# Kernel optimization log

Measured on AMD Instinct MI355X. Metric: run time of the kernel, lower is better.

The kernel has to match this reference:

```python
import jax, jax.numpy as jnp
import numpy as np

B, S, D, H, K = 8, 1024, 512, 512, 8  # batch, seq, input_dim, hidden, max neighbors


def setup_inputs() -> dict:
    key = jax.random.key(0)
    ks = jax.random.split(key, 10)
    p = lambda k, shape: (0.05 * jax.random.normal(k, shape, jnp.float32))
    return {
        "input_t": jax.random.normal(ks[0], (B, S, D), jnp.float32),
        "comb_idx": jax.random.randint(ks[1], (B, S, K), 0, S, jnp.int32),
        "comb_mask": jax.random.randint(ks[2], (B, S, K), 0, 2, jnp.int32),
        "order": jnp.arange(B, dtype=jnp.int64),
        # PyTorch LSTM params per direction; b = b_ih + b_hh fused (mathematically identical)
        "w_ih_f": p(ks[3], (4 * H, D)),
        "w_hh_f": p(ks[4], (4 * H, H)),
        "b_f": p(ks[5], (4 * H,)),
        "w_ih_b": p(ks[6], (4 * H, D)),
        "w_hh_b": p(ks[7], (4 * H, H)),
        "b_b": p(ks[8], (4 * H,)),
    }


def _lstm_scan(x_sbd, w_ih, w_hh, b, reverse):
    # x_sbd: [S, B, D]; PyTorch gate order i, f, g, o; zero initial state (inithidden)
    Bb = x_sbd.shape[1]
    Hh = w_hh.shape[1]
    h0 = jnp.zeros((Bb, Hh), x_sbd.dtype)
    c0 = jnp.zeros((Bb, Hh), x_sbd.dtype)

    def cell(carry, xt):
        h, c = carry
        z = xt @ w_ih.T + h @ w_hh.T + b
        i, f, g, o = jnp.split(z, 4, axis=-1)
        c = jax.nn.sigmoid(f) * c + jax.nn.sigmoid(i) * jnp.tanh(g)
        h = jax.nn.sigmoid(o) * jnp.tanh(c)
        return (h, c), h

    (hn, cn), hs = jax.lax.scan(cell, (h0, c0), x_sbd, reverse=reverse)
    return hs, hn, cn  # hs in original time order even when reverse=True


def reference(input_t, comb_idx, comb_mask, order, w_ih_f, w_hh_f, b_f, w_ih_b, w_hh_b, b_b):
    x = jnp.swapaxes(input_t, 0, 1)  # [S, B, D]
    hs_f, hn_f, cn_f = _lstm_scan(x, w_ih_f, w_hh_f, b_f, reverse=False)
    hs_b, hn_b, cn_b = _lstm_scan(x, w_ih_b, w_hh_b, b_b, reverse=True)
    padded = jnp.swapaxes(jnp.concatenate([hs_f, hs_b], axis=-1), 0, 1)  # [B, S, 2H]
    h_n = jnp.stack([hn_f, hn_b])  # [2, B, H]
    c_n = jnp.stack([cn_f, cn_b])

    # comb = batch_comb[order[idx]]
    ci = comb_idx[order]                                  # [B, S, K]
    cm = comb_mask[order].astype(padded.dtype)            # [B, S, K]
    gathered = jax.vmap(lambda xb, ib: xb[ib])(padded, ci)  # [B, S, K, 2H]
    neigh_sum = (gathered * cm[..., None]).sum(axis=2)    # [B, S, 2H]
    cnt = cm.sum(axis=-1)                                 # [B, S]
    rep = (padded + neigh_sum) / (1.0 + cnt)[..., None]   # (x_i + sum_j x_j) / (|comb_i| + 1)
    rep = rep[:, 1:-1, :]                                 # drop first/last token

    # reorder_batch_encoder_rep[order[i]] = rep[i]
    out = jnp.zeros_like(rep).at[order].set(rep)
    return out, h_n, c_n
```

## Files before the change

### kernel.cpp

```cpp
#include <hip/hip_runtime.h>
#include <stdint.h>

typedef unsigned short u16;
typedef unsigned long long u64;
typedef __attribute__((ext_vector_type(8))) short short8v;
typedef __attribute__((ext_vector_type(4))) float f32x4;

#define OUT_HN   8372224
#define OUT_CN   8380416

#define WS_WIH0  0
#define WS_WIH1  (WS_WIH0 + 2097152)
#define WS_WHH0  (WS_WIH1 + 2097152)
#define WS_WHH1  (WS_WHH0 + 2097152)
#define WS_HSB0  (WS_WHH1 + 2097152)
#define WS_HSB1  (WS_HSB0 + 8396800)
#define WS_FLAGS (WS_HSB1 + 8396800)

__device__ __forceinline__ u16 f2bf(float f) {
  uint32_t u = __float_as_uint(f);
  u += 0x7FFFu + ((u >> 16) & 1u);
  return (u16)(u >> 16);
}
__device__ __forceinline__ float bf2f(u16 v) {
  return __uint_as_float(((uint32_t)v) << 16);
}

__global__ void k_f2bf(const float* __restrict__ src, u16* __restrict__ dst, int n) {
  int i = blockIdx.x * blockDim.x + threadIdx.x;
  int stride = gridDim.x * blockDim.x;
  for (; i < n; i += stride) dst[i] = f2bf(src[i]);
}

__global__ void k_init(uint32_t* flags) {
  if (threadIdx.x < 64) flags[threadIdx.x] = 0;
}

__launch_bounds__(256, 1)
__global__ void k_lstm(const float* __restrict__ xf,
                       const u16* __restrict__ wih0, const u16* __restrict__ wih1,
                       const u16* __restrict__ whh0, const u16* __restrict__ whh1,
                       const float* __restrict__ bias0, const float* __restrict__ bias1,
                       u16* hsb0, u16* hsb1, float* out, uint32_t* flags)
{
  const int tid  = threadIdx.x;
  const int wid  = tid >> 6;
  const int lane = tid & 63;
  const int dir  = blockIdx.x >> 4;
  const int wg   = blockIdx.x & 15;
  const int jbase = wg * 32;

  const u16*  wih  = dir ? wih1  : wih0;
  const u16*  whh  = dir ? whh1  : whh0;
  const float* bias = dir ? bias1 : bias0;
  u16* hsb = dir ? hsb1 : hsb0;
  uint32_t* fl = flags + dir * 16;

  __shared__ u16 hL[8 * 512];
  __shared__ u16 xL[8 * 512];
  __shared__ float zL[4 * 8 * 32];
  __shared__ u16 hS[8 * 32];

  short8v bih[2][16], bhh[2][16];
  {
    const int rr = lane & 15;
    const int ko = (lane >> 4) * 8;
    #pragma unroll
    for (int nt = 0; nt < 2; ++nt) {
      const int row = wid * 512 + jbase + nt * 16 + rr;
      #pragma unroll
      for (int kt = 0; kt < 16; ++kt) {
        bih[nt][kt] = *(const short8v*)(wih + (size_t)row * 512 + kt * 32 + ko);
        bhh[nt][kt] = *(const short8v*)(whh + (size_t)row * 512 + kt * 32 + ko);
      }
    }
  }

  const int cb = tid >> 5;
  const int cj = tid & 31;
  float c_state = 0.f;
  const float bz0 = bias[0 * 512 + jbase + cj];
  const float bz1 = bias[1 * 512 + jbase + cj];
  const float bz2 = bias[2 * 512 + jbase + cj];
  const float bz3 = bias[3 * 512 + jbase + cj];

  const int rB = lane & 7;
  const int q  = lane >> 4;

  const f32x4 fzero = {0.f, 0.f, 0.f, 0.f};
  f32x4 acc0 = fzero, acc1 = fzero;

  #define STAGE_X(tcol)                                                        \
    {                                                                          \
      _Pragma("unroll")                                                        \
      for (int half = 0; half < 2; ++half) {                                   \
        int g = tid + half * 256;                                              \
        int r = g >> 6, B = g & 63;                                            \
        const float* xr = xf + ((size_t)r * 1024 + (tcol)) * 512 + B * 8;      \
        float4 a = *(const float4*)xr;                                         \
        float4 b = *(const float4*)(xr + 4);                                   \
        short8v v;                                                             \
        v[0] = (short)f2bf(a.x); v[1] = (short)f2bf(a.y);                      \
        v[2] = (short)f2bf(a.z); v[3] = (short)f2bf(a.w);                      \
        v[4] = (short)f2bf(b.x); v[5] = (short)f2bf(b.y);                      \
        v[6] = (short)f2bf(b.z); v[7] = (short)f2bf(b.w);                      \
        *(short8v*)(xL + r * 512 + ((B ^ r) << 3)) = v;                        \
      }                                                                        \
    }

  {
    const int t0 = dir ? 1023 : 0;
    STAGE_X(t0);
    __syncthreads();
    #pragma unroll
    for (int kt = 0; kt < 16; ++kt) {
      short8v ax = *(const short8v*)(xL + rB * 512 + (((kt * 4 + q) ^ rB) << 3));
      acc0 = __builtin_amdgcn_mfma_f32_16x16x32_bf16(ax, bih[0][kt], acc0, 0, 0, 0);
      acc1 = __builtin_amdgcn_mfma_f32_16x16x32_bf16(ax, bih[1][kt], acc1, 0, 0, 0);
    }
  }

  for (int step = 0; step < 1024; ++step) {
    if (step > 0) {
      if (tid < 16) {
        int guard = 0;
        while (__hip_atomic_load(&fl[tid], __ATOMIC_RELAXED, __HIP_MEMORY_SCOPE_AGENT)
               < (uint32_t)step && ++guard < (1 << 15)) { }
      }
      __syncthreads();
      {
        const u64* hc = (const u64*)(hsb + (size_t)step * 4096);
        u64 d0 = __hip_atomic_load(hc + 4 * tid + 0, __ATOMIC_RELAXED, __HIP_MEMORY_SCOPE_AGENT);
        u64 d1 = __hip_atomic_load(hc + 4 * tid + 1, __ATOMIC_RELAXED, __HIP_MEMORY_SCOPE_AGENT);
        u64 d2 = __hip_atomic_load(hc + 4 * tid + 2, __ATOMIC_RELAXED, __HIP_MEMORY_SCOPE_AGENT);
        u64 d3 = __hip_atomic_load(hc + 4 * tid + 3, __ATOMIC_RELAXED, __HIP_MEMORY_SCOPE_AGENT);
        union { u64 qq[2]; short8v v; } p0, p1;
        p0.qq[0] = d0; p0.qq[1] = d1;
        p1.qq[0] = d2; p1.qq[1] = d3;
        int G0 = 2 * tid, G1 = 2 * tid + 1;
        int r0 = G0 >> 6, B0 = G0 & 63;
        int r1 = G1 >> 6, B1 = G1 & 63;
        *(short8v*)(hL + r0 * 512 + ((B0 ^ r0) << 3)) = p0.v;
        *(short8v*)(hL + r1 * 512 + ((B1 ^ r1) << 3)) = p1.v;
      }
      __syncthreads();
      #pragma unroll
      for (int kt = 0; kt < 16; ++kt) {
        short8v ah = *(const short8v*)(hL + rB * 512 + (((kt * 4 + q) ^ rB) << 3));
        acc0 = __builtin_amdgcn_mfma_f32_16x16x32_bf16(ah, bhh[0][kt], acc0, 0, 0, 0);
        acc1 = __builtin_amdgcn_mfma_f32_16x16x32_bf16(ah, bhh[1][kt], acc1, 0, 0, 0);
      }
    }
    if (lane < 32) {
      #pragma unroll
      for (int r = 0; r < 4; ++r) {
        const int brow = (lane >> 4) * 4 + r;
        zL[wid * 256 + brow * 32 + (lane & 15)]      = acc0[r];
        zL[wid * 256 + brow * 32 + 16 + (lane & 15)] = acc1[r];
      }
    }
    __syncthreads();
    {
      float zi = zL[0 * 256 + cb * 32 + cj] + bz0;
      float zf = zL[1 * 256 + cb * 32 + cj] + bz1;
      float zg = zL[2 * 256 + cb * 32 + cj] + bz2;
      float zo = zL[3 * 256 + cb * 32 + cj] + bz3;
      float si = 1.f / (1.f + __expf(-zi));
      float sf = 1.f / (1.f + __expf(-zf));
      float so = 1.f / (1.f + __expf(-zo));
      float ag = fabsf(zg); float eg = __expf(-2.f * ag);
      float tg = (1.f - eg) / (1.f + eg); tg = copysignf(tg, zg);
      c_state = sf * c_state + si * tg;
      float ac = fabsf(c_state); float ec = __expf(-2.f * ac);
      float tc = (1.f - ec) / (1.f + ec); tc = copysignf(tc, c_state);
      float h = so * tc;
      hS[cb * 32 + cj] = f2bf(h);
      if (step == 1023) {
        out[OUT_HN + dir * 4096 + cb * 512 + jbase + cj] = h;
        out[OUT_CN + dir * 4096 + cb * 512 + jbase + cj] = c_state;
      }
    }
    __syncthreads();
    if (tid < 64) {
      const int pb = tid >> 3;
      const int pt = tid & 7;
      u64 hv = *(const u64*)(hS + pb * 32 + 4 * pt);
      u64* dst = (u64*)(hsb + ((size_t)(step + 1) * 8 + pb) * 512 + jbase + 4 * pt);
      __hip_atomic_store(dst, hv, __ATOMIC_RELAXED, __HIP_MEMORY_SCOPE_AGENT);
      asm volatile("s_waitcnt vmcnt(0)" ::: "memory");
    }
    if (tid == 0) {
      __hip_atomic_store(&fl[wg], (uint32_t)(step + 1), __ATOMIC_RELAXED,
                         __HIP_MEMORY_SCOPE_AGENT);
    }
    if (step < 1023) {
      acc0 = fzero; acc1 = fzero;
      const int tn = dir ? (1022 - step) : (step + 1);
      STAGE_X(tn);
      __syncthreads();
      #pragma unroll
      for (int kt = 0; kt < 16; ++kt) {
        short8v ax = *(const short8v*)(xL + rB * 512 + (((kt * 4 + q) ^ rB) << 3));
        acc0 = __builtin_amdgcn_mfma_f32_16x16x32_bf16(ax, bih[0][kt], acc0, 0, 0, 0);
        acc1 = __builtin_amdgcn_mfma_f32_16x16x32_bf16(ax, bih[1][kt], acc1, 0, 0, 0);
      }
    }
  }
}

__global__ void k_combine(const u16* __restrict__ hsb0, const u16* __restrict__ hsb1,
                          const int* __restrict__ cidx, const int* __restrict__ cmask,
                          const int* __restrict__ order, float* __restrict__ out)
{
  const int tid = threadIdx.x;
  const int b = blockIdx.x / 1022;
  const int s = 1 + (blockIdx.x % 1022);
  __shared__ int sidx[8];
  __shared__ float smask[8];
  __shared__ int rsh;
  if (tid == 0) rsh = order[b];
  __syncthreads();
  const int r = rsh;
  if (tid < 8) {
    size_t base = ((size_t)r * 1024 + s) * 8 + tid;
    sidx[tid] = cidx[base];
    smask[tid] = (float)cmask[base];
  }
  __syncthreads();
  float cnt = 0.f;
  #pragma unroll
  for (int k = 0; k < 8; ++k) cnt += smask[k];
  const float inv = 1.f / (1.f + cnt);

  const int col0 = tid * 4;
  const bool isF = col0 < 512;
  const int cloc = isF ? col0 : col0 - 512;
  const u16* hb = isF ? hsb0 : hsb1;

  float v0, v1, v2, v3;
  {
    size_t ci2 = isF ? (size_t)(s + 1) : (size_t)(1024 - s);
    ushort4 qv = *(const ushort4*)(hb + (ci2 * 8 + b) * 512 + cloc);
    v0 = bf2f(qv.x); v1 = bf2f(qv.y); v2 = bf2f(qv.z); v3 = bf2f(qv.w);
  }
  #pragma unroll
  for (int k = 0; k < 8; ++k) {
    float m = smask[k];
    if (m != 0.f) {
      int sp = sidx[k];
      size_t ci2 = isF ? (size_t)(sp + 1) : (size_t)(1024 - sp);
      ushort4 qv = *(const ushort4*)(hb + (ci2 * 8 + b) * 512 + cloc);
      v0 += m * bf2f(qv.x); v1 += m * bf2f(qv.y); v2 += m * bf2f(qv.z); v3 += m * bf2f(qv.w);
    }
  }
  size_t ob = ((size_t)r * 1022 + (s - 1)) * 1024 + col0;
  float4 ov; ov.x = v0 * inv; ov.y = v1 * inv; ov.z = v2 * inv; ov.w = v3 * inv;
  *(float4*)(out + ob) = ov;
}

extern "C" void kernel_launch(void* const* d_in, const int* in_sizes, int n_in,
                              void* d_out, int out_size, void* d_ws, size_t ws_size,
                              hipStream_t stream)
{
  const float* x      = (const float*)d_in[0];
  const int*   cidx   = (const int*)d_in[1];
  const int*   cmask  = (const int*)d_in[2];
  const int*   order  = (const int*)d_in[3];
  const float* wihf = (const float*)d_in[4];
  const float* whhf = (const float*)d_in[5];
  const float* bf   = (const float*)d_in[6];
  const float* wihb = (const float*)d_in[7];
  const float* whhb = (const float*)d_in[8];
  const float* bb   = (const float*)d_in[9];
  float* out = (float*)d_out;

  char* ws = (char*)d_ws;
  u16* WIH0 = (u16*)(ws + WS_WIH0);
  u16* WIH1 = (u16*)(ws + WS_WIH1);
  u16* WHH0 = (u16*)(ws + WS_WHH0);
  u16* WHH1 = (u16*)(ws + WS_WHH1);
  u16* HSB0 = (u16*)(ws + WS_HSB0);
  u16* HSB1 = (u16*)(ws + WS_HSB1);
  uint32_t* FLAGS = (uint32_t*)(ws + WS_FLAGS);

  hipLaunchKernelGGL(k_f2bf, dim3(256), dim3(256), 0, stream, wihf, WIH0, 2048 * 512);
  hipLaunchKernelGGL(k_f2bf, dim3(256), dim3(256), 0, stream, wihb, WIH1, 2048 * 512);
  hipLaunchKernelGGL(k_f2bf, dim3(256), dim3(256), 0, stream, whhf, WHH0, 2048 * 512);
  hipLaunchKernelGGL(k_f2bf, dim3(256), dim3(256), 0, stream, whhb, WHH1, 2048 * 512);
  hipLaunchKernelGGL(k_init, dim3(1), dim3(64), 0, stream, FLAGS);
  hipLaunchKernelGGL(k_lstm, dim3(32), dim3(256), 0, stream,
                     x, WIH0, WIH1, WHH0, WHH1, bf, bb, HSB0, HSB1, out, FLAGS);
  hipLaunchKernelGGL(k_combine, dim3(8 * 1022), dim3(256), 0, stream,
                     HSB0, HSB1, cidx, cmask, order, out);
}
```

Before: 3.353 ms.

## Precompute input projections in parallel kernel, keep only recurrent matmul in sequential loop

Moves the x·W_ih projection out of the sequential LSTM loop into a separate highly parallel kernel (k_zx) that writes bf16 pre-activations to workspace. The recurrent kernel then only does h·W_hh per step plus a small load of the precomputed gates, shortening the critical path per timestep. Weight bf16 conversion kernels are removed and fused into the register loads. It adds a large workspace buffer, bf16 rounding of the input gate contributions, and possibly segmented launches if workspace is small.

```diff
diff --git a/kernel.cpp b/kernel.cpp
--- a/kernel.cpp
+++ b/kernel.cpp
@@ -9,13 +9,11 @@
 #define OUT_HN   8372224
 #define OUT_CN   8380416
 
-#define WS_WIH0  0
-#define WS_WIH1  (WS_WIH0 + 2097152)
-#define WS_WHH0  (WS_WIH1 + 2097152)
-#define WS_WHH1  (WS_WHH0 + 2097152)
-#define WS_HSB0  (WS_WHH1 + 2097152)
-#define WS_HSB1  (WS_HSB0 + 8396800)
-#define WS_FLAGS (WS_HSB1 + 8396800)
+#define WS_FLAGS 0
+#define WS_CSB   4096
+#define WS_HSB0  36864
+#define WS_HSB1  8433664
+#define WS_ZX    16830464
 
 __device__ __forceinline__ u16 f2bf(float f) {
   uint32_t u = __float_as_uint(f);
@@ -25,23 +23,122 @@
 __device__ __forceinline__ float bf2f(u16 v) {
   return __uint_as_float(((uint32_t)v) << 16);
 }
-
-__global__ void k_f2bf(const float* __restrict__ src, u16* __restrict__ dst, int n) {
-  int i = blockIdx.x * blockDim.x + threadIdx.x;
-  int stride = gridDim.x * blockDim.x;
-  for (; i < n; i += stride) dst[i] = f2bf(src[i]);
+__device__ __forceinline__ short8v cvt8(const float* p) {
+  float4 a = *(const float4*)p;
+  float4 b = *(const float4*)(p + 4);
+  short8v r;
+  r[0] = (short)f2bf(a.x); r[1] = (short)f2bf(a.y);
+  r[2] = (short)f2bf(a.z); r[3] = (short)f2bf(a.w);
+  r[4] = (short)f2bf(b.x); r[5] = (short)f2bf(b.y);
+  r[6] = (short)f2bf(b.z); r[7] = (short)f2bf(b.w);
+  return r;
 }
 
 __global__ void k_init(uint32_t* flags) {
   if (threadIdx.x < 64) flags[threadIdx.x] = 0;
 }
 
+__global__ void k_zero(u16* h0, u16* h1, float* c) {
+  int i = blockIdx.x * blockDim.x + threadIdx.x;
+  if (i < 4096) { h0[i] = 0; h1[i] = 0; }
+  if (i < 8192) c[i] = 0.f;
+}
+
+#define STAGE_X(tcol)                                                          \
+  {                                                                            \
+    _Pragma("unroll")                                                          \
+    for (int half = 0; half < 2; ++half) {                                     \
+      int g = tid + half * 256;                                                \
+      int r = g >> 6, B = g & 63;                                              \
+      const float* xr = xf + ((size_t)r * 1024 + (tcol)) * 512 + B * 8;        \
+      float4 a = *(const float4*)xr;                                           \
+      float4 b = *(const float4*)(xr + 4);                                     \
+      short8v v;                                                               \
+      v[0] = (short)f2bf(a.x); v[1] = (short)f2bf(a.y);                        \
+      v[2] = (short)f2bf(a.z); v[3] = (short)f2bf(a.w);                        \
+      v[4] = (short)f2bf(b.x); v[5] = (short)f2bf(b.y);                        \
+      v[6] = (short)f2bf(b.z); v[7] = (short)f2bf(b.w);                        \
+      *(short8v*)(xL + r * 512 + ((B ^ r) << 3)) = v;                          \
+    }                                                                          \
+  }
+
+__global__ void k_zx(const float* __restrict__ xf,
+                     const float* __restrict__ wihf, const float* __restrict__ wihb,
+                     u16* __restrict__ zx, int s0, int seglen)
+{
+  const int nch  = seglen >> 5;
+  const int bid  = blockIdx.x;
+  const int chunk = bid % nch;
+  const int wg   = (bid / nch) & 15;
+  const int dir  = bid / (nch * 16);
+  const int tid  = threadIdx.x;
+  const int wid  = tid >> 6;
+  const int lane = tid & 63;
+  const int jbase = wg * 32;
+  const float* wih = dir ? wihb : wihf;
+
+  __shared__ u16 xL[8 * 512];
+  __shared__ float zL[4 * 8 * 32];
+
+  short8v bih[2][16];
+  {
+    const int rr = lane & 15;
+    const int ko = (lane >> 4) * 8;
+    #pragma unroll
+    for (int nt = 0; nt < 2; ++nt) {
+      const int row = wid * 512 + jbase + nt * 16 + rr;
+      #pragma unroll
+      for (int kt = 0; kt < 16; ++kt)
+        bih[nt][kt] = cvt8(wih + (size_t)row * 512 + kt * 32 + ko);
+    }
+  }
+
+  const int rB = lane & 7;
+  const int q  = lane >> 4;
+  const f32x4 fzero = {0.f, 0.f, 0.f, 0.f};
+
+  for (int i = 0; i < 32; ++i) {
+    const int sidx = chunk * 32 + i;
+    const int gstep = s0 + sidx;
+    const int tn = dir ? (1023 - gstep) : gstep;
+    STAGE_X(tn);
+    __syncthreads();
+    f32x4 acc0 = fzero, acc1 = fzero;
+    #pragma unroll
+    for (int kt = 0; kt < 16; ++kt) {
+      short8v ax = *(const short8v*)(xL + rB * 512 + (((kt * 4 + q) ^ rB) << 3));
+      acc0 = __builtin_amdgcn_mfma_f32_16x16x32_bf16(ax, bih[0][kt], acc0, 0, 0, 0);
+      acc1 = __builtin_amdgcn_mfma_f32_16x16x32_bf16(ax, bih[1][kt], acc1, 0, 0, 0);
+    }
+    if (lane < 32) {
+      #pragma unroll
+      for (int r = 0; r < 4; ++r) {
+        const int brow = (lane >> 4) * 4 + r;
+        zL[wid * 256 + brow * 32 + (lane & 15)]      = acc0[r];
+        zL[wid * 256 + brow * 32 + 16 + (lane & 15)] = acc1[r];
+      }
+    }
+    __syncthreads();
+    if (tid < 128) {
+      const int b = tid >> 4;
+      const int r = (tid & 15) * 8;
+      const int g = r >> 5;
+      const int jj = r & 31;
+      short8v v;
+      #pragma unroll
+      for (int w = 0; w < 8; ++w) v[w] = (short)f2bf(zL[g * 256 + b * 32 + jj + w]);
+      *(short8v*)(zx + (((size_t)dir * seglen + sidx) * 16 + wg) * 1024 + tid * 8) = v;
+    }
+    __syncthreads();
+  }
+}
+
 __launch_bounds__(256, 1)
-__global__ void k_lstm(const float* __restrict__ xf,
-                       const u16* __restrict__ wih0, const u16* __restrict__ wih1,
-                       const u16* __restrict__ whh0, const u16* __restrict__ whh1,
+__global__ void k_lstm(const float* __restrict__ whhf, const float* __restrict__ whhb,
                        const float* __restrict__ bias0, const float* __restrict__ bias1,
-                       u16* hsb0, u16* hsb1, float* out, uint32_t* flags)
+                       const u16* __restrict__ zx,
+                       u16* hsb0, u16* hsb1, float* csb, float* out,
+                       uint32_t* flags, int s0, int s1, int seglen)
 {
   const int tid  = threadIdx.x;
   const int wid  = tid >> 6;
@@ -50,18 +147,17 @@
   const int wg   = blockIdx.x & 15;
   const int jbase = wg * 32;
 
-  const u16*  wih  = dir ? wih1  : wih0;
-  const u16*  whh  = dir ? whh1  : whh0;
+  const float* whh  = dir ? whhb : whhf;
   const float* bias = dir ? bias1 : bias0;
   u16* hsb = dir ? hsb1 : hsb0;
   uint32_t* fl = flags + dir * 16;
 
   __shared__ u16 hL[8 * 512];
-  __shared__ u16 xL[8 * 512];
   __shared__ float zL[4 * 8 * 32];
   __shared__ u16 hS[8 * 32];
-
-  short8v bih[2][16], bhh[2][16];
+  __shared__ u64 zxL[256];
+
+  short8v bhh[2][16];
   {
     const int rr = lane & 15;
     const int ko = (lane >> 4) * 8;
@@ -69,87 +165,58 @@
     for (int nt = 0; nt < 2; ++nt) {
       const int row = wid * 512 + jbase + nt * 16 + rr;
       #pragma unroll
-      for (int kt = 0; kt < 16; ++kt) {
-        bih[nt][kt] = *(const short8v*)(wih + (size_t)row * 512 + kt * 32 + ko);
-        bhh[nt][kt] = *(const short8v*)(whh + (size_t)row * 512 + kt * 32 + ko);
-      }
+      for (int kt = 0; kt < 16; ++kt)
+        bhh[nt][kt] = cvt8(whh + (size_t)row * 512 + kt * 32 + ko);
     }
   }
 
   const int cb = tid >> 5;
   const int cj = tid & 31;
-  float c_state = 0.f;
   const float bz0 = bias[0 * 512 + jbase + cj];
   const float bz1 = bias[1 * 512 + jbase + cj];
   const float bz2 = bias[2 * 512 + jbase + cj];
   const float bz3 = bias[3 * 512 + jbase + cj];
+  float* cp = csb + dir * 4096 + cb * 512 + jbase + cj;
+  float c_state = *cp;
 
   const int rB = lane & 7;
   const int q  = lane >> 4;
-
   const f32x4 fzero = {0.f, 0.f, 0.f, 0.f};
-  f32x4 acc0 = fzero, acc1 = fzero;
-
-  #define STAGE_X(tcol)                                                        \
-    {                                                                          \
-      _Pragma("unroll")                                                        \
-      for (int half = 0; half < 2; ++half) {                                   \
-        int g = tid + half * 256;                                              \
-        int r = g >> 6, B = g & 63;                                            \
-        const float* xr = xf + ((size_t)r * 1024 + (tcol)) * 512 + B * 8;      \
-        float4 a = *(const float4*)xr;                                         \
-        float4 b = *(const float4*)(xr + 4);                                   \
-        short8v v;                                                             \
-        v[0] = (short)f2bf(a.x); v[1] = (short)f2bf(a.y);                      \
-        v[2] = (short)f2bf(a.z); v[3] = (short)f2bf(a.w);                      \
-        v[4] = (short)f2bf(b.x); v[5] = (short)f2bf(b.y);                      \
-        v[6] = (short)f2bf(b.z); v[7] = (short)f2bf(b.w);                      \
-        *(short8v*)(xL + r * 512 + ((B ^ r) << 3)) = v;                        \
-      }                                                                        \
-    }
-
-  {
-    const int t0 = dir ? 1023 : 0;
-    STAGE_X(t0);
-    __syncthreads();
+  const u16* zx16 = (const u16*)zxL;
+
+  for (int gstep = s0; gstep < s1; ++gstep) {
+    {
+      const u64* zp = (const u64*)(zx + (((size_t)dir * seglen + (gstep - s0)) * 16 + wg) * 1024);
+      zxL[tid] = zp[tid];
+    }
+    if (tid < 16) {
+      int guard = 0;
+      while (__hip_atomic_load(&fl[tid], __ATOMIC_RELAXED, __HIP_MEMORY_SCOPE_AGENT)
+             < (uint32_t)gstep && ++guard < (1 << 15)) { }
+    }
+    __syncthreads();
+    {
+      const u64* hc = (const u64*)(hsb + (size_t)gstep * 4096);
+      u64 d0 = __hip_atomic_load(hc + 4 * tid + 0, __ATOMIC_RELAXED, __HIP_MEMORY_SCOPE_AGENT);
+      u64 d1 = __hip_atomic_load(hc + 4 * tid + 1, __ATOMIC_RELAXED, __HIP_MEMORY_SCOPE_AGENT);
+      u64 d2 = __hip_atomic_load(hc + 4 * tid + 2, __ATOMIC_RELAXED, __HIP_MEMORY_SCOPE_AGENT);
+      u64 d3 = __hip_atomic_load(hc + 4 * tid + 3, __ATOMIC_RELAXED, __HIP_MEMORY_SCOPE_AGENT);
+      union { u64 qq[2]; short8v v; } p0, p1;
+      p0.qq[0] = d0; p0.qq[1] = d1;
+      p1.qq[0] = d2; p1.qq[1] = d3;
+      int G0 = 2 * tid, G1 = 2 * tid + 1;
+      int r0 = G0 >> 6, B0 = G0 & 63;
+      int r1 = G1 >> 6, B1 = G1 & 63;
+      *(short8v*)(hL + r0 * 512 + ((B0 ^ r0) << 3)) = p0.v;
+      *(short8v*)(hL + r1 * 512 + ((B1 ^ r1) << 3)) = p1.v;
+    }
+    __syncthreads();
+    f32x4 acc0 = fzero, acc1 = fzero;
     #pragma unroll
     for (int kt = 0; kt < 16; ++kt) {
-      short8v ax = *(const short8v*)(xL + rB * 512 + (((kt * 4 + q) ^ rB) << 3));
-      acc0 = __builtin_amdgcn_mfma_f32_16x16x32_bf16(ax, bih[0][kt], acc0, 0, 0, 0);
-      acc1 = __builtin_amdgcn_mfma_f32_16x16x32_bf16(ax, bih[1][kt], acc1, 0, 0, 0);
-    }
-  }
-
-  for (int step = 0; step < 1024; ++step) {
-    if (step > 0) {
-      if (tid < 16) {
-        int guard = 0;
-        while (__hip_atomic_load(&fl[tid], __ATOMIC_RELAXED, __HIP_MEMORY_SCOPE_AGENT)
-               < (uint32_t)step && ++guard < (1 << 15)) { }
-      }
-      __syncthreads();
-      {
-        const u64* hc = (const u64*)(hsb + (size_t)step * 4096);
-        u64 d0 = __hip_atomic_load(hc + 4 * tid + 0, __ATOMIC_RELAXED, __HIP_MEMORY_SCOPE_AGENT);
-        u64 d1 = __hip_atomic_load(hc + 4 * tid + 1, __ATOMIC_RELAXED, __HIP_MEMORY_SCOPE_AGENT);
-        u64 d2 = __hip_atomic_load(hc + 4 * tid + 2, __ATOMIC_RELAXED, __HIP_MEMORY_SCOPE_AGENT);
-        u64 d3 = __hip_atomic_load(hc + 4 * tid + 3, __ATOMIC_RELAXED, __HIP_MEMORY_SCOPE_AGENT);
-        union { u64 qq[2]; short8v v; } p0, p1;
-        p0.qq[0] = d0; p0.qq[1] = d1;
-        p1.qq[0] = d2; p1.qq[1] = d3;
-        int G0 = 2 * tid, G1 = 2 * tid + 1;
-        int r0 = G0 >> 6, B0 = G0 & 63;
-        int r1 = G1 >> 6, B1 = G1 & 63;
-        *(short8v*)(hL + r0 * 512 + ((B0 ^ r0) << 3)) = p0.v;
-        *(short8v*)(hL + r1 * 512 + ((B1 ^ r1) << 3)) = p1.v;
-      }
-      __syncthreads();
-      #pragma unroll
-      for (int kt = 0; kt < 16; ++kt) {
-        short8v ah = *(const short8v*)(hL + rB * 512 + (((kt * 4 + q) ^ rB) << 3));
-        acc0 = __builtin_amdgcn_mfma_f32_16x16x32_bf16(ah, bhh[0][kt], acc0, 0, 0, 0);
-        acc1 = __builtin_amdgcn_mfma_f32_16x16x32_bf16(ah, bhh[1][kt], acc1, 0, 0, 0);
-      }
+      short8v ah = *(const short8v*)(hL + rB * 512 + (((kt * 4 + q) ^ rB) << 3));
+      acc0 = __builtin_amdgcn_mfma_f32_16x16x32_bf16(ah, bhh[0][kt], acc0, 0, 0, 0);
+      acc1 = __builtin_amdgcn_mfma_f32_16x16x32_bf16(ah, bhh[1][kt], acc1, 0, 0, 0);
     }
     if (lane < 32) {
       #pragma unroll
@@ -161,10 +228,10 @@
     }
     __syncthreads();
     {
-      float zi = zL[0 * 256 + cb * 32 + cj] + bz0;
-      float zf = zL[1 * 256 + cb * 32 + cj] + bz1;
-      float zg = zL[2 * 256 + cb * 32 + cj] + bz2;
-      float zo = zL[3 * 256 + cb * 32 + cj] + bz3;
+      float zi = zL[0 * 256 + cb * 32 + cj] + bz0 + bf2f(zx16[cb * 128 +  0 + cj]);
+      float zf = zL[1 * 256 + cb * 32 + cj] + bz1 + bf2f(zx16[cb * 128 + 32 + cj]);
+      float zg = zL[2 * 256 + cb * 32 + cj] + bz2 + bf2f(zx16[cb * 128 + 64 + cj]);
+      float zo = zL[3 * 256 + cb * 32 + cj] + bz3 + bf2f(zx16[cb * 128 + 96 + cj]);
       float si = 1.f / (1.f + __expf(-zi));
       float sf = 1.f / (1.f + __expf(-zf));
       float so = 1.f / (1.f + __expf(-zo));
@@ -175,7 +242,7 @@
       float tc = (1.f - ec) / (1.f + ec); tc = copysignf(tc, c_state);
       float h = so * tc;
       hS[cb * 32 + cj] = f2bf(h);
-      if (step == 1023) {
+      if (gstep == 1023) {
         out[OUT_HN + dir * 4096 + cb * 512 + jbase + cj] = h;
         out[OUT_CN + dir * 4096 + cb * 512 + jbase + cj] = c_state;
       }
@@ -185,27 +252,16 @@
       const int pb = tid >> 3;
       const int pt = tid & 7;
       u64 hv = *(const u64*)(hS + pb * 32 + 4 * pt);
-      u64* dst = (u64*)(hsb + ((size_t)(step + 1) * 8 + pb) * 512 + jbase + 4 * pt);
+      u64* dst = (u64*)(hsb + ((size_t)(gstep + 1) * 8 + pb) * 512 + jbase + 4 * pt);
       __hip_atomic_store(dst, hv, __ATOMIC_RELAXED, __HIP_MEMORY_SCOPE_AGENT);
       asm volatile("s_waitcnt vmcnt(0)" ::: "memory");
     }
     if (tid == 0) {
-      __hip_atomic_store(&fl[wg], (uint32_t)(step + 1), __ATOMIC_RELAXED,
+      __hip_atomic_store(&fl[wg], (uint32_t)(gstep + 1), __ATOMIC_RELAXED,
                          __HIP_MEMORY_SCOPE_AGENT);
     }
-    if (step < 1023) {
-      acc0 = fzero; acc1 = fzero;
-      const int tn = dir ? (1022 - step) : (step + 1);
-      STAGE_X(tn);
-      __syncthreads();
-      #pragma unroll
-      for (int kt = 0; kt < 16; ++kt) {
-        short8v ax = *(const short8v*)(xL + rB * 512 + (((kt * 4 + q) ^ rB) << 3));
-        acc0 = __builtin_amdgcn_mfma_f32_16x16x32_bf16(ax, bih[0][kt], acc0, 0, 0, 0);
-        acc1 = __builtin_amdgcn_mfma_f32_16x16x32_bf16(ax, bih[1][kt], acc1, 0, 0, 0);
-      }
-    }
-  }
+  }
+  *cp = c_state;
 }
 
 __global__ void k_combine(const u16* __restrict__ hsb0, const u16* __restrict__ hsb1,
@@ -275,21 +331,25 @@
   float* out = (float*)d_out;
 
   char* ws = (char*)d_ws;
-  u16* WIH0 = (u16*)(ws + WS_WIH0);
-  u16* WIH1 = (u16*)(ws + WS_WIH1);
-  u16* WHH0 = (u16*)(ws + WS_WHH0);
-  u16* WHH1 = (u16*)(ws + WS_WHH1);
+  uint32_t* FLAGS = (uint32_t*)(ws + WS_FLAGS);
+  float* CSB = (float*)(ws + WS_CSB);
   u16* HSB0 = (u16*)(ws + WS_HSB0);
   u16* HSB1 = (u16*)(ws + WS_HSB1);
-  uint32_t* FLAGS = (uint32_t*)(ws + WS_FLAGS);
-
-  hipLaunchKernelGGL(k_f2bf, dim3(256), dim3(256), 0, stream, wihf, WIH0, 2048 * 512);
-  hipLaunchKernelGGL(k_f2bf, dim3(256), dim3(256), 0, stream, wihb, WIH1, 2048 * 512);
-  hipLaunchKernelGGL(k_f2bf, dim3(256), dim3(256), 0, stream, whhf, WHH0, 2048 * 512);
-  hipLaunchKernelGGL(k_f2bf, dim3(256), dim3(256), 0, stream, whhb, WHH1, 2048 * 512);
+  u16* ZX   = (u16*)(ws + WS_ZX);
+
+  const int seglen = (ws_size >= (size_t)WS_ZX + 1024ull * 65536) ? 1024 : 128;
+
   hipLaunchKernelGGL(k_init, dim3(1), dim3(64), 0, stream, FLAGS);
-  hipLaunchKernelGGL(k_lstm, dim3(32), dim3(256), 0, stream,
-                     x, WIH0, WIH1, WHH0, WHH1, bf, bb, HSB0, HSB1, out, FLAGS);
+  hipLaunchKernelGGL(k_zero, dim3(32), dim3(256), 0, stream, HSB0, HSB1, CSB);
+
+  for (int s0 = 0; s0 < 1024; s0 += seglen) {
+    hipLaunchKernelGGL(k_zx, dim3(2 * 16 * (seglen >> 5)), dim3(256), 0, stream,
+                       x, wihf, wihb, ZX, s0, seglen);
+    hipLaunchKernelGGL(k_lstm, dim3(32), dim3(256), 0, stream,
+                       whhf, whhb, bf, bb, ZX, HSB0, HSB1, CSB, out, FLAGS,
+                       s0, s0 + seglen, seglen);
+  }
+
   hipLaunchKernelGGL(k_combine, dim3(8 * 1022), dim3(256), 0, stream,
                      HSB0, HSB1, cidx, cmask, order, out);
 }
```

After: 2.974 ms. -11.3%, faster.
